# Performance work log

Hardware: AMD Instinct MI355X
Metric: run time of the kernel (lower is better)

## Reference

```python
import jax, jax.numpy as jnp
import numpy as np

B, N, D, H = 4, 2048, 512, 8
HD = D // H  # 64


def setup_inputs() -> dict:
    key = jax.random.key(0)
    ks = jax.random.split(key, 12)
    s = 0.02
    return {
        "x": jax.random.normal(ks[0], (B, N, D), jnp.float32),
        "freqs": jax.random.normal(ks[1], (B, N, HD // 2), jnp.float32),
        # weights stored as (in, out); torch Linear applies x @ W.T + b
        "wqkv_w": jax.random.normal(ks[2], (D, 3 * D), jnp.float32) * s,
        "wqkv_b": jax.random.normal(ks[3], (3 * D,), jnp.float32) * s,
        "out_w": jax.random.normal(ks[4], (D, D), jnp.float32) * s,
        "out_b": jax.random.normal(ks[5], (D,), jnp.float32) * s,
        "ffn1_w": jax.random.normal(ks[6], (2 * D, 2 * D), jnp.float32) * s,
        "ffn1_b": jax.random.normal(ks[7], (2 * D,), jnp.float32) * s,
        "ln_g": jnp.ones((2 * D,), jnp.float32),
        "ln_b": jnp.zeros((2 * D,), jnp.float32),
        "ffn2_w": jax.random.normal(ks[8], (2 * D, D), jnp.float32) * s,
        "ffn2_b": jax.random.normal(ks[9], (D,), jnp.float32) * s,
    }


def _rope(t, cos, sin):
    # t: [B,H,N,HD]; cos/sin: [B,1,N,HD/2]
    x1, x2 = t[..., ::2], t[..., 1::2]
    return jnp.stack([x1 * cos - x2 * sin, x1 * sin + x2 * cos], axis=-1).reshape(t.shape)


def reference(x, freqs, wqkv_w, wqkv_b, out_w, out_b,
              ffn1_w, ffn1_b, ln_g, ln_b, ffn2_w, ffn2_b):
    b, n, d = x.shape
    h, hd = H, d // H
    qkv = x @ wqkv_w + wqkv_b                      # [B,N,3D]
    q, k, v = jnp.split(qkv, 3, axis=-1)
    to_heads = lambda t: t.reshape(b, n, h, hd).transpose(0, 2, 1, 3)  # [B,H,N,HD]
    q, k, v = to_heads(q), to_heads(k), to_heads(v)
    cos = jnp.cos(freqs)[:, None]                  # [B,1,N,HD/2]
    sin = jnp.sin(freqs)[:, None]
    q = _rope(q, cos, sin)
    k = _rope(k, cos, sin)
    scale = hd ** -0.5
    attn = jax.nn.softmax(jnp.einsum('bhqd,bhkd->bhqk', q, k) * scale, axis=-1)
    msg = jnp.einsum('bhqk,bhkd->bhqd', attn, v).transpose(0, 2, 1, 3).reshape(b, n, d)
    msg = msg @ out_w + out_b
    # FFN on concat([x, msg]): Linear -> LayerNorm -> GELU(exact) -> Linear
    hcat = jnp.concatenate([x, msg], axis=-1) @ ffn1_w + ffn1_b   # [B,N,2D]
    mu = hcat.mean(-1, keepdims=True)
    var = hcat.var(-1, keepdims=True)
    hcat = (hcat - mu) * jax.lax.rsqrt(var + 1e-5) * ln_g + ln_b
    hcat = jax.nn.gelu(hcat, approximate=False)
    return x + hcat @ ffn2_w + ffn2_b
```

## Files before the change

### kernel.cpp

```cpp
#include <hip/hip_runtime.h>
#include <hip/hip_bf16.h>
#include <math.h>

typedef __bf16 bf16;
typedef __bf16 bf16x2 __attribute__((ext_vector_type(2)));
typedef __bf16 bf16x4 __attribute__((ext_vector_type(4)));
typedef __bf16 bf16x8 __attribute__((ext_vector_type(8)));
typedef float f32x4 __attribute__((ext_vector_type(4)));
typedef float f32x16 __attribute__((ext_vector_type(16)));

#define MFMA16(a, b, c) __builtin_amdgcn_mfma_f32_16x16x32_bf16(a, b, c, 0, 0, 0)
#define MFMA32(a, b, c) __builtin_amdgcn_mfma_f32_32x32x16_bf16(a, b, c, 0, 0, 0)


__global__ __launch_bounds__(256) void prep_kernel(
    const float* __restrict__ wqkv_w, const float* __restrict__ out_w,
    const float* __restrict__ ffn1_w, const float* __restrict__ ffn2_w,
    const float* __restrict__ x, const float* __restrict__ freqs,
    const float* __restrict__ ffn1_b, const float* __restrict__ out_b,
    bf16* __restrict__ wqkv_t, bf16* __restrict__ ffn2_t,
    bf16* __restrict__ fused_t, bf16* __restrict__ ffn1bt,
    bf16* __restrict__ out_cast, bf16* __restrict__ cat,
    float* __restrict__ bias_f, unsigned* __restrict__ tab)
{
    const int bid = blockIdx.x, tid = threadIdx.x;
    __shared__ bf16 tile[32][33];
    __shared__ float red[256];
    if (bid >= 6672) {
        int i = (bid - 6672) * 1024 + tid * 4;
        const float4 f = *(const float4*)(&freqs[i]);
        float s0, c0, s1, c1, s2, c2, s3, c3;
        __sincosf(f.x, &s0, &c0); __sincosf(f.y, &s1, &c1);
        __sincosf(f.z, &s2, &c2); __sincosf(f.w, &s3, &c3);
        union { bf16x2 h2; unsigned u; } p0, p1, p2, p3;
        p0.h2[0] = (bf16)c0; p0.h2[1] = (bf16)s0;
        p1.h2[0] = (bf16)c1; p1.h2[1] = (bf16)s1;
        p2.h2[0] = (bf16)c2; p2.h2[1] = (bf16)s2;
        p3.h2[0] = (bf16)c3; p3.h2[1] = (bf16)s3;
        uint4 o = {p0.u, p1.u, p2.u, p3.u};
        *(uint4*)(&tab[i]) = o;
        return;
    }
    if (bid >= 6656) {
        const int n = (bid - 6656) * 64 + (tid & 63);
        const int ic = tid >> 6;
        float acc = 0.f;
#pragma unroll 8
        for (int i = ic * 128; i < ic * 128 + 128; i++)
            acc += out_b[i] * ffn1_w[(size_t)(512 + i) * 1024 + n];
        red[tid] = acc;
        __syncthreads();
        if (tid < 64)
            bias_f[n] = ffn1_b[n] + red[tid] + red[tid + 64] + red[tid + 128] + red[tid + 192];
        return;
    }
    if (bid >= 2560) {
        int i = (bid - 2560) * 256 + tid;
        int row = i >> 7, col = (i & 127) << 2;
        const float4 v = *(const float4*)(&x[(size_t)row * 512 + col]);
        bf16x4 o; o[0] = (bf16)v.x; o[1] = (bf16)v.y; o[2] = (bf16)v.z; o[3] = (bf16)v.w;
        *(bf16x4*)(&cat[(size_t)row * 1024 + col]) = o;
        return;
    }
    if (bid >= 2304) {
        int i = (bid - 2304) * 1024 + tid * 4;
        const float4 v = *(const float4*)(&out_w[i]);
        bf16x4 o; o[0] = (bf16)v.x; o[1] = (bf16)v.y; o[2] = (bf16)v.z; o[3] = (bf16)v.w;
        *(bf16x4*)(&out_cast[i]) = o;
        return;
    }
    const float* src; bf16* dst; int C, ldd, bx, by;
    if (bid < 768)       { src = wqkv_w;            dst = wqkv_t;  C = 1536; ldd = 512;  int r = bid;        bx = r % 48; by = r / 48; }
    else if (bid < 1280) { src = ffn2_w;            dst = ffn2_t;  C = 512;  ldd = 1024; int r = bid - 768;  bx = r % 16; by = r / 16; }
    else if (bid < 1792) { src = ffn1_w;            dst = fused_t; C = 1024; ldd = 1024; int r = bid - 1280; bx = r % 32; by = r / 32; }
    else                 { src = ffn1_w + 512*1024; dst = ffn1bt;  C = 1024; ldd = 512;  int r = bid - 1792; bx = r % 32; by = r / 32; }
    const int tx = tid & 31, ty = tid >> 5;
    const int xx = bx * 32 + tx;
#pragma unroll
    for (int j = 0; j < 4; j++)
        tile[ty + 8 * j][tx] = (bf16)src[(size_t)(by * 32 + ty + 8 * j) * C + xx];
    __syncthreads();
    const int x2 = by * 32 + tx;
#pragma unroll
    for (int j = 0; j < 4; j++)
        dst[(size_t)(bx * 32 + ty + 8 * j) * ldd + x2] = tile[tx][ty + 8 * j];
}

__global__ __launch_bounds__(256) void qkv_wcomb_kernel(
    const bf16* __restrict__ cat, const bf16* __restrict__ wqkv_t,
    const float* __restrict__ wqkv_b, const unsigned* __restrict__ tab,
    bf16* __restrict__ qbuf, bf16* __restrict__ kbuf, bf16* __restrict__ vbuf,
    const bf16* __restrict__ ffn1bt, const bf16* __restrict__ out_cast,
    bf16* __restrict__ fused_t)
{
    const int bid = blockIdx.x;
    const bool isqkv = bid < 768;
    const bf16* A; const bf16* Bt; int lda, m0, n0;
    if (isqkv) { A = cat;    lda = 1024; Bt = wqkv_t;   n0 = (bid % 12) * 128; m0 = (bid / 12) * 128; }
    else       { int r = bid - 768;
                 A = ffn1bt; lda = 512;  Bt = out_cast; n0 = (r & 3) * 128;    m0 = (r >> 2) * 128; }
    const int K = 512;

    const int tid = threadIdx.x;
    const int lane = tid & 63, wave = tid >> 6;
    const int wm = wave >> 1, wn = wave & 1;
    const int l15 = lane & 15, quad = lane >> 4;

    __shared__ __align__(16) char smem[16384];
    bf16* As = (bf16*)smem;
    bf16* Bs = (bf16*)(smem + 8192);
    unsigned* tabs = (unsigned*)smem;

    const int c0 = tid, c1 = tid + 256;
    const int r0 = c0 >> 2, kc0 = (c0 & 3) << 3;
    const int r1 = c1 >> 2, kc1 = (c1 & 3) << 3;
    const bf16* pA0 = &A[(size_t)(m0 + r0) * lda + kc0];
    const bf16* pA1 = &A[(size_t)(m0 + r1) * lda + kc1];
    const bf16* pB0 = &Bt[(size_t)(n0 + r0) * K + kc0];
    const bf16* pB1 = &Bt[(size_t)(n0 + r1) * K + kc1];

    const f32x4 zero = {0.f, 0.f, 0.f, 0.f};
    f32x4 acc[4][4];
#pragma unroll
    for (int i = 0; i < 4; i++)
#pragma unroll
        for (int j = 0; j < 4; j++) acc[i][j] = zero;

    bf16x8 ra0 = *(const bf16x8*)pA0;
    bf16x8 ra1 = *(const bf16x8*)pA1;
    bf16x8 rb0 = *(const bf16x8*)pB0;
    bf16x8 rb1 = *(const bf16x8*)pB1;

    for (int k0 = 0; k0 < K; k0 += 32) {
        __syncthreads();
        *(bf16x8*)(&As[c0 * 8]) = ra0;
        *(bf16x8*)(&As[c1 * 8]) = ra1;
        *(bf16x8*)(&Bs[c0 * 8]) = rb0;
        *(bf16x8*)(&Bs[c1 * 8]) = rb1;
        __syncthreads();
        if (k0 + 32 < K) {
            ra0 = *(const bf16x8*)(pA0 + k0 + 32);
            ra1 = *(const bf16x8*)(pA1 + k0 + 32);
            rb0 = *(const bf16x8*)(pB0 + k0 + 32);
            rb1 = *(const bf16x8*)(pB1 + k0 + 32);
        }
        bf16x8 af[4], bfv[4];
#pragma unroll
        for (int t = 0; t < 4; t++) {
            af[t]  = *(const bf16x8*)(&As[(wm * 64 + t * 16 + l15) * 32 + quad * 8]);
            bfv[t] = *(const bf16x8*)(&Bs[(wn * 64 + t * 16 + l15) * 32 + quad * 8]);
        }
#pragma unroll
        for (int mt = 0; mt < 4; mt++)
#pragma unroll
            for (int nt = 0; nt < 4; nt++)
                acc[mt][nt] = MFMA16(af[mt], bfv[nt], acc[mt][nt]);
    }

    const int row_base = m0 + wm * 64;
    const int col_base = n0 + wn * 64;

    if (isqkv) {
        const int sector = col_base >> 9;
        const bool dorope = sector < 2;
        if (dorope) {
            __syncthreads();
#pragma unroll
            for (int ps = 0; ps < 4; ps++) {
                int idx = ps * 1024 + tid * 4;
                *(uint4*)(&tabs[idx]) = *(const uint4*)(&tab[(size_t)m0 * 32 + idx]);
            }
            __syncthreads();
        }
        const float SCQ = 0.125f * 1.44269504089f;
        bf16* dstbase = (sector == 0) ? qbuf : (sector == 1 ? kbuf : vbuf);
#pragma unroll
        for (int nt = 0; nt < 4; nt++) {
            const int col = col_base + nt * 16 + l15;
            const int cq = col & 511;
            const int h = cq >> 6, hd = cq & 63;
            const float bv = wqkv_b[col];
            const int ihalf = hd >> 1;
            const bool odd = (hd & 1) != 0;
#pragma unroll
            for (int mt = 0; mt < 4; mt++) {
#pragma unroll
                for (int r = 0; r < 4; r++) {
                    const int mrow = row_base + mt * 16 + quad * 4 + r;
                    float v = acc[mt][nt][r] + bv;
                    float o = v;
                    if (dorope) {
                        float p = __shfl_xor(v, 1);
                        const int rl = wm * 64 + mt * 16 + quad * 4 + r;
                        union { unsigned u; bf16x2 h2; } t2;
                        t2.u = tabs[rl * 32 + ihalf];
                        float cs = t2.h2[0], sn = t2.h2[1];
                        o = odd ? (p * sn + v * cs) : (v * cs - p * sn);
                        if (sector == 0) o *= SCQ;
                    }
                    const int b = mrow >> 11, n = mrow & 2047;
                    dstbase[(((size_t)b * 8 + h) * 2048 + n) * 64 + hd] = (bf16)o;
                }
            }
        }
    } else {
#pragma unroll
        for (int nt = 0; nt < 4; nt++) {
            const int col = col_base + nt * 16 + l15;
#pragma unroll
            for (int mt = 0; mt < 4; mt++) {
#pragma unroll
                for (int r = 0; r < 4; r++) {
                    const int row = row_base + mt * 16 + quad * 4 + r;
                    fused_t[(size_t)row * 1024 + 512 + col] = (bf16)acc[mt][nt][r];
                }
            }
        }
    }
}

template <int MODE>
__global__ __launch_bounds__(256) void gemm64_mfma(
    const bf16* __restrict__ A, int lda, const bf16* __restrict__ Bt,
    const float* __restrict__ bias, void* __restrict__ outv,
    const float* __restrict__ auxf, int K)
{
    const int tid = threadIdx.x;
    const int lane = tid & 63, wave = tid >> 6;
    const int l15 = lane & 15, quad = lane >> 4;
    const int m0 = blockIdx.y * 128;
    const int n0 = blockIdx.x * 64;

    __shared__ bf16 As[128 * 32];
    __shared__ bf16 Bs[64 * 32];

    const int c0 = tid, c1 = tid + 256;
    const int ar0 = c0 >> 2, akc0 = (c0 & 3) << 3;
    const int ar1 = c1 >> 2, akc1 = (c1 & 3) << 3;
    const int br0 = tid >> 2, bkc0 = (tid & 3) << 3;
    const bf16* pA0 = &A[(size_t)(m0 + ar0) * lda + akc0];
    const bf16* pA1 = &A[(size_t)(m0 + ar1) * lda + akc1];
    const bf16* pB0 = &Bt[(size_t)(n0 + br0) * K + bkc0];

    const f32x4 zero = {0.f, 0.f, 0.f, 0.f};
    f32x4 acc[2][4];
#pragma unroll
    for (int i = 0; i < 2; i++)
#pragma unroll
        for (int j = 0; j < 4; j++) acc[i][j] = zero;

    bf16x8 ra0 = *(const bf16x8*)pA0;
    bf16x8 ra1 = *(const bf16x8*)pA1;
    bf16x8 rb0 = *(const bf16x8*)pB0;

    for (int k0 = 0; k0 < K; k0 += 32) {
        __syncthreads();
        *(bf16x8*)(&As[c0 * 8]) = ra0;
        *(bf16x8*)(&As[c1 * 8]) = ra1;
        *(bf16x8*)(&Bs[tid * 8]) = rb0;
        __syncthreads();
        if (k0 + 32 < K) {
            ra0 = *(const bf16x8*)(pA0 + k0 + 32);
            ra1 = *(const bf16x8*)(pA1 + k0 + 32);
            rb0 = *(const bf16x8*)(pB0 + k0 + 32);
        }
        bf16x8 af[2], bfv[4];
#pragma unroll
        for (int t = 0; t < 2; t++)
            af[t] = *(const bf16x8*)(&As[(wave * 32 + t * 16 + l15) * 32 + quad * 8]);
#pragma unroll
        for (int t = 0; t < 4; t++)
            bfv[t] = *(const bf16x8*)(&Bs[(t * 16 + l15) * 32 + quad * 8]);
#pragma unroll
        for (int mt = 0; mt < 2; mt++)
#pragma unroll
            for (int nt = 0; nt < 4; nt++)
                acc[mt][nt] = MFMA16(af[mt], bfv[nt], acc[mt][nt]);
    }

    const int row_base = m0 + wave * 32;
#pragma unroll
    for (int nt = 0; nt < 4; nt++) {
        const int col = n0 + nt * 16 + l15;
        const float bv = bias[col];
#pragma unroll
        for (int mt = 0; mt < 2; mt++) {
#pragma unroll
            for (int r = 0; r < 4; r++) {
                const int row = row_base + mt * 16 + quad * 4 + r;
                float v = acc[mt][nt][r] + bv;
                if constexpr (MODE == 2) {
                    ((bf16*)outv)[(size_t)row * 1024 + col] = (bf16)v;
                } else {
                    v += auxf[(size_t)row * 512 + col];
                    ((float*)outv)[(size_t)row * 512 + col] = v;
                }
            }
        }
    }
}

__global__ __launch_bounds__(512) void attn_kernel(const bf16* __restrict__ qb,
                                                   const bf16* __restrict__ kb,
                                                   const bf16* __restrict__ vb,
                                                   bf16* __restrict__ cat)
{
    __shared__ __align__(16) char smem[53248];
    bf16* Ks   = (bf16*)smem;
    bf16* Vts0 = (bf16*)(smem + 18432);
    bf16* Vts1 = (bf16*)(smem + 35840);

    const int tid = threadIdx.x, lane = tid & 63, wave = tid >> 6;
    const int l31 = lane & 31, half = lane >> 5;
    const int qg = wave >> 2, kh = wave & 3;
    const int bh = blockIdx.x >> 5, qt = blockIdx.x & 31;
    const int b = bh >> 3, h = bh & 7;
    const size_t base = (size_t)bh * 2048 * 64;
    const int m0 = qt * 64 + qg * 32;

    bf16x8 aq[4];
#pragma unroll
    for (int k4 = 0; k4 < 4; k4++)
        aq[k4] = *(const bf16x8*)(&qb[base + (size_t)(m0 + l31) * 64 + k4 * 16 + half * 8]);

    f32x16 accO[2];
#pragma unroll
    for (int i = 0; i < 16; i++) { accO[0][i] = 0.f; accO[1][i] = 0.f; }
    float lsum = 0.f;

    int krow[2], kcol[2];
#pragma unroll
    for (int i = 0; i < 2; i++) { int c = tid + i * 512; krow[i] = c >> 3; kcol[i] = (c & 7) << 3; }
    const int vpr = tid & 63, vdg = tid >> 6;

    bf16x8 kreg[2], vr0, vr1;
    auto prefetch = [&](int key0) {
#pragma unroll
        for (int i = 0; i < 2; i++)
            kreg[i] = *(const bf16x8*)(&kb[base + (size_t)(key0 + krow[i]) * 64 + kcol[i]]);
        vr0 = *(const bf16x8*)(&vb[base + (size_t)(key0 + 2 * vpr) * 64 + vdg * 8]);
        vr1 = *(const bf16x8*)(&vb[base + (size_t)(key0 + 2 * vpr + 1) * 64 + vdg * 8]);
    };

    const int ko = kh * 32;
    union Bu { bf16x8 v; unsigned u[4]; };
    Bu B0p, B1p;
    auto pv = [&](const bf16* Vr) {
#pragma unroll
        for (int dh = 0; dh < 2; dh++) {
            bf16x8 av0 = *(const bf16x8*)(&Vr[(dh * 32 + l31) * 136 + ko + half * 8]);
            bf16x8 av1 = *(const bf16x8*)(&Vr[(dh * 32 + l31) * 136 + ko + 16 + half * 8]);
            accO[dh] = MFMA32(av0, B0p.v, accO[dh]);
            accO[dh] = MFMA32(av1, B1p.v, accO[dh]);
        }
    };

    prefetch(0);
#pragma unroll
    for (int kt = 0; kt < 16; kt++) {
        bf16* Vw = (kt & 1) ? Vts1 : Vts0;
        bf16* Vr = (kt & 1) ? Vts0 : Vts1;
        __syncthreads();
#pragma unroll
        for (int i = 0; i < 2; i++)
            *(bf16x8*)(&Ks[krow[i] * 72 + kcol[i]]) = kreg[i];
#pragma unroll
        for (int j = 0; j < 8; j++) {
            bf16x2 pr; pr[0] = vr0[j]; pr[1] = vr1[j];
            *(bf16x2*)(&Vw[(vdg * 8 + j) * 136 + 2 * vpr]) = pr;
        }
        __syncthreads();
        if (kt < 15) prefetch((kt + 1) * 128);

        f32x16 s;
#pragma unroll
        for (int i = 0; i < 16; i++) s[i] = 0.f;
#pragma unroll
        for (int k4 = 0; k4 < 4; k4++) {
            bf16x8 ak = *(const bf16x8*)(&Ks[(ko + l31) * 72 + k4 * 16 + half * 8]);
            s = MFMA32(ak, aq[k4], s);
        }
        if (kt > 0) pv(Vr);
        float p[16];
#pragma unroll
        for (int r = 0; r < 16; r++) p[r] = __builtin_amdgcn_exp2f(s[r]);
        lsum += (((p[0] + p[1]) + (p[2] + p[3])) + ((p[4] + p[5]) + (p[6] + p[7])))
              + (((p[8] + p[9]) + (p[10] + p[11])) + ((p[12] + p[13]) + (p[14] + p[15])));
        unsigned pk[8];
#pragma unroll
        for (int i2 = 0; i2 < 8; i2++) {
            union { bf16x2 hh; unsigned u; } t;
            t.hh[0] = (bf16)p[2 * i2]; t.hh[1] = (bf16)p[2 * i2 + 1];
            pk[i2] = t.u;
        }
        const unsigned sa = half ? pk[0] : pk[2];
        const unsigned sb = half ? pk[1] : pk[3];
        const unsigned sc2 = half ? pk[4] : pk[6];
        const unsigned sd = half ? pk[5] : pk[7];
        const unsigned ra = (unsigned)__shfl_xor((int)sa, 32);
        const unsigned rb = (unsigned)__shfl_xor((int)sb, 32);
        const unsigned rc = (unsigned)__shfl_xor((int)sc2, 32);
        const unsigned rd = (unsigned)__shfl_xor((int)sd, 32);
        B0p.u[0] = half ? ra : pk[0];
        B0p.u[1] = half ? rb : pk[1];
        B0p.u[2] = half ? pk[2] : ra;
        B0p.u[3] = half ? pk[3] : rb;
        B1p.u[0] = half ? rc : pk[4];
        B1p.u[1] = half ? rd : pk[5];
        B1p.u[2] = half ? pk[6] : rc;
        B1p.u[3] = half ? pk[7] : rd;
    }
    pv(Vts1);

    auto slotp = [&](int s2) { return (float*)smem + ((s2 * 2 + qg) * 64 + lane) * 33; };
    __syncthreads();
    if (kh == 1 || kh == 3) {
        float* pr2 = slotp(kh >> 1);
#pragma unroll
        for (int dh = 0; dh < 2; dh++)
#pragma unroll
            for (int r = 0; r < 16; r++) pr2[dh * 16 + r] = accO[dh][r];
        pr2[32] = lsum;
    }
    __syncthreads();
    if (kh == 0 || kh == 2) {
        float* pr2 = slotp(kh >> 1);
#pragma unroll
        for (int dh = 0; dh < 2; dh++)
#pragma unroll
            for (int r = 0; r < 16; r++) accO[dh][r] += pr2[dh * 16 + r];
        lsum += pr2[32];
    }
    __syncthreads();
    if (kh == 2) {
        float* pr2 = slotp(0);
#pragma unroll
        for (int dh = 0; dh < 2; dh++)
#pragma unroll
            for (int r = 0; r < 16; r++) pr2[dh * 16 + r] = accO[dh][r];
        pr2[32] = lsum;
    }
    __syncthreads();
    if (kh == 0) {
        float* pr2 = slotp(0);
#pragma unroll
        for (int dh = 0; dh < 2; dh++)
#pragma unroll
            for (int r = 0; r < 16; r++) accO[dh][r] += pr2[dh * 16 + r];
        lsum += pr2[32];
        lsum += __shfl_xor(lsum, 32);
        const float inv = 1.0f / lsum;
        const int n = m0 + l31;
        bf16* aor = cat + ((size_t)b * 2048 + n) * 1024 + 512 + h * 64;
#pragma unroll
        for (int dh = 0; dh < 2; dh++) {
#pragma unroll
            for (int g = 0; g < 4; g++) {
                bf16x4 o4;
#pragma unroll
                for (int e = 0; e < 4; e++) o4[e] = (bf16)(accO[dh][g * 4 + e] * inv);
                *(bf16x4*)(&aor[dh * 32 + g * 8 + half * 4]) = o4;
            }
        }
    }
}

__global__ __launch_bounds__(256) void ln_gelu_kernel(bf16* __restrict__ hb,
                                                      const float* __restrict__ g,
                                                      const float* __restrict__ bt)
{
    const int row = blockIdx.x, tid = threadIdx.x;
    const int lane = tid & 63, wave = tid >> 6;
    bf16* hr = hb + (size_t)row * 1024;
    bf16x4 hv = *(const bf16x4*)(&hr[tid * 4]);
    float v0 = hv[0], v1 = hv[1], v2 = hv[2], v3 = hv[3];
    float s = v0 + v1 + v2 + v3;
    float q = v0 * v0 + v1 * v1 + v2 * v2 + v3 * v3;
    for (int o = 32; o; o >>= 1) { s += __shfl_xor(s, o); q += __shfl_xor(q, o); }
    __shared__ float red[8];
    if (lane == 0) { red[wave] = s; red[4 + wave] = q; }
    __syncthreads();
    s = red[0] + red[1] + red[2] + red[3];
    q = red[4] + red[5] + red[6] + red[7];
    const float mu = s * (1.f / 1024.f);
    const float rstd = rsqrtf(q * (1.f / 1024.f) - mu * mu + 1e-5f);
    const float4 gv = *(const float4*)(&g[tid * 4]);
    const float4 bv = *(const float4*)(&bt[tid * 4]);
    float vv[4] = {v0, v1, v2, v3};
    const float gg[4] = {gv.x, gv.y, gv.z, gv.w};
    const float bb[4] = {bv.x, bv.y, bv.z, bv.w};
    bf16x4 o4;
#pragma unroll
    for (int i = 0; i < 4; i++) {
        float y = (vv[i] - mu) * rstd * gg[i] + bb[i];
        float t = 1.5957691216f * y * (1.0f + 0.044715f * y * y);
        float e = __builtin_amdgcn_exp2f(-1.44269504089f * t);
        o4[i] = (bf16)(y * __builtin_amdgcn_rcpf(1.0f + e));
    }
    *(bf16x4*)(&hr[tid * 4]) = o4;
}

extern "C" void kernel_launch(void* const* d_in, const int* in_sizes, int n_in,
                              void* d_out, int out_size, void* d_ws, size_t ws_size,
                              hipStream_t stream) {
    (void)in_sizes; (void)n_in; (void)out_size; (void)ws_size;
    const float* x      = (const float*)d_in[0];
    const float* freqs  = (const float*)d_in[1];
    const float* wqkv_w = (const float*)d_in[2];
    const float* wqkv_b = (const float*)d_in[3];
    const float* out_w  = (const float*)d_in[4];
    const float* out_b  = (const float*)d_in[5];
    const float* ffn1_w = (const float*)d_in[6];
    const float* ffn1_b = (const float*)d_in[7];
    const float* ln_g   = (const float*)d_in[8];
    const float* ln_b   = (const float*)d_in[9];
    const float* ffn2_w = (const float*)d_in[10];
    const float* ffn2_b = (const float*)d_in[11];
    float* out = (float*)d_out;
    bf16* ws   = (bf16*)d_ws;

    bf16* wqkv_t   = ws;
    bf16* ffn2_t   = wqkv_t + 1536 * 512;
    bf16* fused_t  = ffn2_t + 512 * 1024;
    bf16* ffn1bt   = fused_t + 1024 * 1024;
    bf16* out_cast = ffn1bt + 1024 * 512;
    bf16* cat      = out_cast + 512 * 512;
    bf16* qbuf     = cat + (size_t)8192 * 1024;
    bf16* kbuf     = qbuf + (size_t)8192 * 512;
    bf16* vbuf     = kbuf + (size_t)8192 * 512;
    float* bias_f  = (float*)(vbuf + (size_t)8192 * 512);
    unsigned* tab  = (unsigned*)(bias_f + 1024);
    bf16* hbuf     = qbuf;

    prep_kernel<<<6928, 256, 0, stream>>>(wqkv_w, out_w, ffn1_w, ffn2_w, x, freqs,
                                          ffn1_b, out_b,
                                          wqkv_t, ffn2_t, fused_t, ffn1bt, out_cast, cat,
                                          bias_f, tab);
    qkv_wcomb_kernel<<<800, 256, 0, stream>>>(cat, wqkv_t, wqkv_b, tab, qbuf, kbuf, vbuf,
                                              ffn1bt, out_cast, fused_t);
    attn_kernel<<<1024, 512, 0, stream>>>(qbuf, kbuf, vbuf, cat);
    gemm64_mfma<2><<<dim3(16, 64), 256, 0, stream>>>(cat, 1024, fused_t, bias_f, hbuf, nullptr, 1024);
    ln_gelu_kernel<<<8192, 256, 0, stream>>>(hbuf, ln_g, ln_b);
    gemm64_mfma<3><<<dim3(8, 64), 256, 0, stream>>>(hbuf, 1024, ffn2_t, ffn2_b, out, x, 1024);
}
```

Measured before the change: 261.4 us.

## Enlarge FFN GEMM tiles to 128x128 with K=64 steps and padded LDS

The two FFN GEMMs now use 128x128 output tiles per block with a 2x2 wave layout, each wave computing 64x64. The K step doubles to 64 and LDS rows are padded to 72 elements to reduce bank conflicts. The goal is more MFMA work per LDS load and fewer global loads per output. In exchange each block uses more registers, and the grid shrinks to 512 and 256 blocks, which may underfill the 256 CUs for the second GEMM.

```diff
diff --git a/kernel.cpp b/kernel.cpp
--- a/kernel.cpp
+++ b/kernel.cpp
@@ -220,80 +220,90 @@
 }
 
 template <int MODE>
-__global__ __launch_bounds__(256) void gemm64_mfma(
+__global__ __launch_bounds__(256) void gemm_mfma(
     const bf16* __restrict__ A, int lda, const bf16* __restrict__ Bt,
     const float* __restrict__ bias, void* __restrict__ outv,
     const float* __restrict__ auxf, int K)
 {
     const int tid = threadIdx.x;
     const int lane = tid & 63, wave = tid >> 6;
+    const int wm = wave >> 1, wn = wave & 1;
     const int l15 = lane & 15, quad = lane >> 4;
     const int m0 = blockIdx.y * 128;
-    const int n0 = blockIdx.x * 64;
-
-    __shared__ bf16 As[128 * 32];
-    __shared__ bf16 Bs[64 * 32];
-
-    const int c0 = tid, c1 = tid + 256;
-    const int ar0 = c0 >> 2, akc0 = (c0 & 3) << 3;
-    const int ar1 = c1 >> 2, akc1 = (c1 & 3) << 3;
-    const int br0 = tid >> 2, bkc0 = (tid & 3) << 3;
-    const bf16* pA0 = &A[(size_t)(m0 + ar0) * lda + akc0];
-    const bf16* pA1 = &A[(size_t)(m0 + ar1) * lda + akc1];
-    const bf16* pB0 = &Bt[(size_t)(n0 + br0) * K + bkc0];
+    const int n0 = blockIdx.x * 128;
+
+    __shared__ bf16 As[128 * 72];
+    __shared__ bf16 Bs[128 * 72];
+
+    int row[4], kc[4];
+    const bf16 *pA[4], *pB[4];
+#pragma unroll
+    for (int i = 0; i < 4; i++) {
+        int c = tid + i * 256;
+        row[i] = c >> 3; kc[i] = (c & 7) << 3;
+        pA[i] = &A[(size_t)(m0 + row[i]) * lda + kc[i]];
+        pB[i] = &Bt[(size_t)(n0 + row[i]) * K + kc[i]];
+    }
 
     const f32x4 zero = {0.f, 0.f, 0.f, 0.f};
-    f32x4 acc[2][4];
-#pragma unroll
-    for (int i = 0; i < 2; i++)
+    f32x4 acc[4][4];
+#pragma unroll
+    for (int i = 0; i < 4; i++)
 #pragma unroll
         for (int j = 0; j < 4; j++) acc[i][j] = zero;
 
-    bf16x8 ra0 = *(const bf16x8*)pA0;
-    bf16x8 ra1 = *(const bf16x8*)pA1;
-    bf16x8 rb0 = *(const bf16x8*)pB0;
-
-    for (int k0 = 0; k0 < K; k0 += 32) {
-        __syncthreads();
-        *(bf16x8*)(&As[c0 * 8]) = ra0;
-        *(bf16x8*)(&As[c1 * 8]) = ra1;
-        *(bf16x8*)(&Bs[tid * 8]) = rb0;
-        __syncthreads();
-        if (k0 + 32 < K) {
-            ra0 = *(const bf16x8*)(pA0 + k0 + 32);
-            ra1 = *(const bf16x8*)(pA1 + k0 + 32);
-            rb0 = *(const bf16x8*)(pB0 + k0 + 32);
-        }
-        bf16x8 af[2], bfv[4];
-#pragma unroll
-        for (int t = 0; t < 2; t++)
-            af[t] = *(const bf16x8*)(&As[(wave * 32 + t * 16 + l15) * 32 + quad * 8]);
-#pragma unroll
-        for (int t = 0; t < 4; t++)
-            bfv[t] = *(const bf16x8*)(&Bs[(t * 16 + l15) * 32 + quad * 8]);
-#pragma unroll
-        for (int mt = 0; mt < 2; mt++)
-#pragma unroll
-            for (int nt = 0; nt < 4; nt++)
-                acc[mt][nt] = MFMA16(af[mt], bfv[nt], acc[mt][nt]);
-    }
-
-    const int row_base = m0 + wave * 32;
+    bf16x8 ra[4], rb[4];
+#pragma unroll
+    for (int i = 0; i < 4; i++) { ra[i] = *(const bf16x8*)pA[i]; rb[i] = *(const bf16x8*)pB[i]; }
+
+    for (int k0 = 0; k0 < K; k0 += 64) {
+        __syncthreads();
+#pragma unroll
+        for (int i = 0; i < 4; i++) {
+            *(bf16x8*)(&As[row[i] * 72 + kc[i]]) = ra[i];
+            *(bf16x8*)(&Bs[row[i] * 72 + kc[i]]) = rb[i];
+        }
+        __syncthreads();
+        if (k0 + 64 < K) {
+#pragma unroll
+            for (int i = 0; i < 4; i++) {
+                ra[i] = *(const bf16x8*)(pA[i] + k0 + 64);
+                rb[i] = *(const bf16x8*)(pB[i] + k0 + 64);
+            }
+        }
+#pragma unroll
+        for (int kk = 0; kk < 2; kk++) {
+            bf16x8 af[4], bfv[4];
+#pragma unroll
+            for (int t = 0; t < 4; t++) {
+                af[t]  = *(const bf16x8*)(&As[(wm * 64 + t * 16 + l15) * 72 + kk * 32 + quad * 8]);
+                bfv[t] = *(const bf16x8*)(&Bs[(wn * 64 + t * 16 + l15) * 72 + kk * 32 + quad * 8]);
+            }
+#pragma unroll
+            for (int mt = 0; mt < 4; mt++)
+#pragma unroll
+                for (int nt = 0; nt < 4; nt++)
+                    acc[mt][nt] = MFMA16(af[mt], bfv[nt], acc[mt][nt]);
+        }
+    }
+
+    const int row_base = m0 + wm * 64;
+    const int col_base = n0 + wn * 64;
 #pragma unroll
     for (int nt = 0; nt < 4; nt++) {
-        const int col = n0 + nt * 16 + l15;
+        const int col = col_base + nt * 16 + l15;
         const float bv = bias[col];
 #pragma unroll
-        for (int mt = 0; mt < 2; mt++) {
+        for (int mt = 0; mt < 4; mt++) {
 #pragma unroll
             for (int r = 0; r < 4; r++) {
-                const int row = row_base + mt * 16 + quad * 4 + r;
+                const int row2 = row_base + mt * 16 + quad * 4 + r;
                 float v = acc[mt][nt][r] + bv;
                 if constexpr (MODE == 2) {
-                    ((bf16*)outv)[(size_t)row * 1024 + col] = (bf16)v;
+                    ((bf16*)outv)[(size_t)row2 * 1024 + col] = (bf16)v;
                 } else {
-                    v += auxf[(size_t)row * 512 + col];
-                    ((float*)outv)[(size_t)row * 512 + col] = v;
+                    v += auxf[(size_t)row2 * 512 + col];
+                    ((float*)outv)[(size_t)row2 * 512 + col] = v;
                 }
             }
         }
@@ -539,7 +549,7 @@
     qkv_wcomb_kernel<<<800, 256, 0, stream>>>(cat, wqkv_t, wqkv_b, tab, qbuf, kbuf, vbuf,
                                               ffn1bt, out_cast, fused_t);
     attn_kernel<<<1024, 512, 0, stream>>>(qbuf, kbuf, vbuf, cat);
-    gemm64_mfma<2><<<dim3(16, 64), 256, 0, stream>>>(cat, 1024, fused_t, bias_f, hbuf, nullptr, 1024);
+    gemm_mfma<2><<<dim3(8, 64), 256, 0, stream>>>(cat, 1024, fused_t, bias_f, hbuf, nullptr, 1024);
     ln_gelu_kernel<<<8192, 256, 0, stream>>>(hbuf, ln_g, ln_b);
-    gemm64_mfma<3><<<dim3(8, 64), 256, 0, stream>>>(hbuf, 1024, ffn2_t, ffn2_b, out, x, 1024);
+    gemm_mfma<3><<<dim3(4, 64), 256, 0, stream>>>(hbuf, 1024, ffn2_t, ffn2_b, out, x, 1024);
 }
```

Result: faster. 246.6 us (-5.7%).
